# Kernel optimization log

Hardware: AMD Instinct MI355X
Metric: run time of the kernel (lower is better)

The kernel has to match this reference:

```python
import jax, jax.numpy as jnp
import numpy as np

VOCAB, D, H = 32000, 4096, 1024
B, S = 256, 256
LN_EPS = 1e-5


def setup_inputs() -> dict:
    key = jax.random.key(0)
    ks = jax.random.split(key, 8)
    return {
        "input_ids": jax.random.randint(ks[0], (B, S), 0, VOCAB),
        "attention_mask": jax.random.randint(ks[1], (B, S), 0, 2).astype(jnp.int32),
        "query_ids": jax.random.randint(ks[2], (1, S), 0, VOCAB),
        "query_mask": jax.random.randint(ks[3], (1, S), 0, 2).astype(jnp.int32),
        "embed": jax.random.normal(ks[4], (VOCAB, D), dtype=jnp.float32) * 0.02,
        "ln_g": jnp.ones((D,), jnp.float32),
        "ln_b": jnp.zeros((D,), jnp.float32),
        "kW1": jax.random.normal(ks[5], (H, D), dtype=jnp.float32) * 0.02,
        "kb1": jnp.zeros((H,), jnp.float32),
        "kW2": jax.random.normal(ks[6], (H, H), dtype=jnp.float32) * 0.02,
        "kb2": jnp.zeros((H,), jnp.float32),
        "qW1": jax.random.normal(ks[7], (H, D), dtype=jnp.float32) * 0.02,
        "qb1": jnp.zeros((H,), jnp.float32),
        "qW2": jax.random.normal(jax.random.fold_in(key, 99), (H, H), dtype=jnp.float32) * 0.02,
        "qb2": jnp.zeros((H,), jnp.float32),
        "k": 5,
    }


def _pool_norm(ids, mask, embed, ln_g, ln_b):
    # embedding gather -> masked mean pool -> LayerNorm
    h = embed[ids]                                  # [B, S, D]
    m = mask.astype(h.dtype)[..., None]             # [B, S, 1]
    pooled = (h * m).sum(axis=1) / (m.sum(axis=1) + 1e-9)  # [B, D]
    mu = pooled.mean(axis=-1, keepdims=True)
    var = ((pooled - mu) ** 2).mean(axis=-1, keepdims=True)
    return (pooled - mu) * jax.lax.rsqrt(var + LN_EPS) * ln_g + ln_b


def _mlp(x, W1, b1, W2, b2):
    return jax.nn.relu(x @ W1.T + b1) @ W2.T + b2


def reference(input_ids, attention_mask, query_ids, query_mask, embed, ln_g, ln_b,
              kW1, kb1, kW2, kb2, qW1, qb1, qW2, qb2, k):
    keys = _mlp(_pool_norm(input_ids, attention_mask, embed, ln_g, ln_b),
                kW1, kb1, kW2, kb2)                 # [B, H]
    query = _mlp(_pool_norm(query_ids, query_mask, embed, ln_g, ln_b),
                 qW1, qb1, qW2, qb2)                # [1, H]
    scores = jax.nn.sigmoid((query @ keys.T)[0])    # [B]
    vals, idx = jax.lax.top_k(scores, k)
    return vals, idx
```

## Files before the change

kernel.cpp:

```cpp
#include <hip/hip_runtime.h>
#include <math.h>

#define DD 4096
#define HH 1024
#define BB 256
#define SS 256

typedef unsigned long long u64;
typedef __attribute__((ext_vector_type(4))) short sv4;
typedef __attribute__((ext_vector_type(8))) short sv8;
typedef __attribute__((ext_vector_type(4))) float f32x4;

__device__ __forceinline__ unsigned short f2bf(float x) {
    union { float f; unsigned u; } c; c.f = x;
    unsigned r = c.u + 0x7FFFu + ((c.u >> 16) & 1u);
    return (unsigned short)(r >> 16);
}
__device__ __forceinline__ float bf2f(unsigned short h) {
    union { unsigned u; float f; } c; c.u = ((unsigned)h) << 16;
    return c.f;
}
__device__ __forceinline__ void split4(const float4& v, sv4& h, sv4& l) {
    unsigned short hx = f2bf(v.x), hy = f2bf(v.y), hz = f2bf(v.z), hw = f2bf(v.w);
    h.x = (short)hx; h.y = (short)hy; h.z = (short)hz; h.w = (short)hw;
    l.x = (short)f2bf(v.x - bf2f(hx)); l.y = (short)f2bf(v.y - bf2f(hy));
    l.z = (short)f2bf(v.z - bf2f(hz)); l.w = (short)f2bf(v.w - bf2f(hw));
}
__device__ __forceinline__ void split8(const float4& a, const float4& b,
                                       sv8& h, sv8& l) {
    sv4 h0, l0, h1, l1;
    split4(a, h0, l0);
    split4(b, h1, l1);
    h.s0 = h0.x; h.s1 = h0.y; h.s2 = h0.z; h.s3 = h0.w;
    h.s4 = h1.x; h.s5 = h1.y; h.s6 = h1.z; h.s7 = h1.w;
    l.s0 = l0.x; l.s1 = l0.y; l.s2 = l0.z; l.s3 = l0.w;
    l.s4 = l1.x; l.s5 = l1.y; l.s6 = l1.z; l.s7 = l1.w;
}

__global__ __launch_bounds__(256) void prep_kernel(
        const int* __restrict__ ids, const int* __restrict__ mask,
        const int* __restrict__ qids, const int* __restrict__ qmask,
        int* __restrict__ SortedOff, int* __restrict__ Count) {
    __shared__ int s_key[256];
    __shared__ int wofs[4];
    int b = blockIdx.x, t = threadIdx.x;
    const int* I = (b < BB) ? ids  + b * SS : qids;
    const int* M = (b < BB) ? mask + b * SS : qmask;
    int id = I[t], m = M[t];
    u64 bal = __ballot(m != 0);
    int lane = t & 63, w = t >> 6;
    if (lane == 0) wofs[w] = __popcll(bal);
    s_key[t] = 0x7FFFFFFF;
    __syncthreads();
    int off = 0;
    #pragma unroll
    for (int i = 0; i < 4; ++i) if (i < w) off += wofs[i];
    int total = wofs[0] + wofs[1] + wofs[2] + wofs[3];
    if (m) s_key[off + __popcll(bal & ((1ull << lane) - 1ull))] = id;
    __syncthreads();
    for (int k = 2; k <= 256; k <<= 1) {
        for (int j = k >> 1; j > 0; j >>= 1) {
            int p = t ^ j;
            int a = s_key[t], c = s_key[p];
            bool dir = ((t & k) == 0);
            bool keepMin = ((t < p) == dir);
            int nv = keepMin ? (a < c ? a : c) : (a > c ? a : c);
            __syncthreads();
            s_key[t] = nv;
            __syncthreads();
        }
    }
    SortedOff[b * 256 + t] = (t < total) ? s_key[t] * DD : 0;
    if (t == 0) Count[b] = total;
}

__global__ __launch_bounds__(64) void pool_kernel(
        const int* __restrict__ SortedOff, const int* __restrict__ Count,
        const float* __restrict__ embed, float* __restrict__ Pooled) {
    __shared__ int s_off[256];
    int bid = blockIdx.x, t = threadIdx.x;
    int doc = bid >> 4, slice = bid & 15;
    int total = Count[doc];
    #pragma unroll
    for (int i = 0; i < 4; ++i) s_off[t + i * 64] = SortedOff[doc * 256 + t + i * 64];
    __syncthreads();
    float inv = 1.0f / ((float)total + 1e-9f);
    int col = (slice << 8) + (t << 2);
    const float* eb = embed + col;
    float ax = 0.f, ay = 0.f, az = 0.f, aw = 0.f;
    int j = 0;
    for (; j + 8 <= total; j += 8) {
        const float4 r0 = *(const float4*)(eb + s_off[j + 0]);
        const float4 r1 = *(const float4*)(eb + s_off[j + 1]);
        const float4 r2 = *(const float4*)(eb + s_off[j + 2]);
        const float4 r3 = *(const float4*)(eb + s_off[j + 3]);
        const float4 r4 = *(const float4*)(eb + s_off[j + 4]);
        const float4 r5 = *(const float4*)(eb + s_off[j + 5]);
        const float4 r6 = *(const float4*)(eb + s_off[j + 6]);
        const float4 r7 = *(const float4*)(eb + s_off[j + 7]);
        ax += ((r0.x + r1.x) + (r2.x + r3.x)) + ((r4.x + r5.x) + (r6.x + r7.x));
        ay += ((r0.y + r1.y) + (r2.y + r3.y)) + ((r4.y + r5.y) + (r6.y + r7.y));
        az += ((r0.z + r1.z) + (r2.z + r3.z)) + ((r4.z + r5.z) + (r6.z + r7.z));
        aw += ((r0.w + r1.w) + (r2.w + r3.w)) + ((r4.w + r5.w) + (r6.w + r7.w));
    }
    for (; j < total; ++j) {
        const float4 r0 = *(const float4*)(eb + s_off[j]);
        ax += r0.x; ay += r0.y; az += r0.z; aw += r0.w;
    }
    *(float4*)(Pooled + (size_t)doc * DD + col) =
        make_float4(ax * inv, ay * inv, az * inv, aw * inv);
}

__global__ __launch_bounds__(256) void ln_split_kernel(
        const float* __restrict__ Pooled, const float* __restrict__ g,
        const float* __restrict__ bb, short* __restrict__ Xh,
        short* __restrict__ Xl, float* __restrict__ Xq) {
    __shared__ float lds4[4];
    int b = blockIdx.x, t = threadIdx.x;
    const float* row = Pooled + (size_t)b * DD;
    float4 v[4];
    float s = 0.f;
    #pragma unroll
    for (int i = 0; i < 4; ++i) {
        v[i] = *(const float4*)(row + (t << 2) + (i << 10));
        s += (v[i].x + v[i].y) + (v[i].z + v[i].w);
    }
    #pragma unroll
    for (int o = 32; o; o >>= 1) s += __shfl_down(s, o);
    int lane = t & 63, w = t >> 6;
    if (lane == 0) lds4[w] = s;
    __syncthreads();
    float mu = (lds4[0] + lds4[1] + lds4[2] + lds4[3]) * (1.0f / DD);
    float q = 0.f;
    #pragma unroll
    for (int i = 0; i < 4; ++i) {
        float dx = v[i].x - mu, dy = v[i].y - mu, dz = v[i].z - mu, dw = v[i].w - mu;
        q += (dx * dx + dy * dy) + (dz * dz + dw * dw);
    }
    __syncthreads();
    #pragma unroll
    for (int o = 32; o; o >>= 1) q += __shfl_down(q, o);
    if (lane == 0) lds4[w] = q;
    __syncthreads();
    float var = (lds4[0] + lds4[1] + lds4[2] + lds4[3]) * (1.0f / DD);
    float sc = 1.0f / sqrtf(var + 1e-5f);
    #pragma unroll
    for (int i = 0; i < 4; ++i) {
        int col = (t << 2) + (i << 10);
        float4 gg = *(const float4*)(g + col);
        float4 bv = *(const float4*)(bb + col);
        float4 o4;
        o4.x = (v[i].x - mu) * sc * gg.x + bv.x;
        o4.y = (v[i].y - mu) * sc * gg.y + bv.y;
        o4.z = (v[i].z - mu) * sc * gg.z + bv.z;
        o4.w = (v[i].w - mu) * sc * gg.w + bv.w;
        if (b < BB) {
            sv4 h, l; split4(o4, h, l);
            *(sv4*)(Xh + (size_t)b * DD + col) = h;
            *(sv4*)(Xl + (size_t)b * DD + col) = l;
        } else {
            *(float4*)(Xq + col) = o4;
        }
    }
}

template <bool CONTRIB>
__device__ void gemm_mfma(
        const short* __restrict__ Ah, const short* __restrict__ Al,
        const float* __restrict__ Wf,
        int ldK, int m0, int n0, int kBase, int Kc, int N,
        float* __restrict__ Pout,
        const float* __restrict__ Qv, float* __restrict__ Contrib, int slot) {
    __shared__ short sAh[128 * 40] __attribute__((aligned(16)));
    __shared__ short sAl[128 * 40] __attribute__((aligned(16)));
    __shared__ short sBh[128 * 40] __attribute__((aligned(16)));
    __shared__ short sBl[128 * 40] __attribute__((aligned(16)));
    int tid = threadIdx.x;
    int lane = tid & 63, wv = tid >> 6;
    int wr = wv >> 1, wc = wv & 1;
    int l15 = lane & 15, grp = lane >> 4, lk = grp << 3;
    int srow = tid >> 1, soff = (tid & 1) << 4;
    f32x4 zero = {0.f, 0.f, 0.f, 0.f};
    f32x4 acc[4][4];
    #pragma unroll
    for (int i = 0; i < 4; ++i)
        #pragma unroll
        for (int j = 0; j < 4; ++j) acc[i][j] = zero;

    for (int k0 = 0; k0 < Kc; k0 += 32) {
        int gk = kBase + k0;
        size_t ga = (size_t)(m0 + srow) * ldK + gk + soff;
        sv8 vah0 = *(const sv8*)(Ah + ga);
        sv8 vah1 = *(const sv8*)(Ah + ga + 8);
        sv8 val0 = *(const sv8*)(Al + ga);
        sv8 val1 = *(const sv8*)(Al + ga + 8);
        const float* wp = Wf + (size_t)(n0 + srow) * ldK + gk + soff;
        float4 w0 = *(const float4*)(wp);
        float4 w1 = *(const float4*)(wp + 4);
        float4 w2 = *(const float4*)(wp + 8);
        float4 w3 = *(const float4*)(wp + 12);
        sv8 bh0, bl0, bh1, bl1;
        split8(w0, w1, bh0, bl0);
        split8(w2, w3, bh1, bl1);
        __syncthreads();
        int so = srow * 40 + soff;
        *(sv8*)(sAh + so) = vah0; *(sv8*)(sAh + so + 8) = vah1;
        *(sv8*)(sAl + so) = val0; *(sv8*)(sAl + so + 8) = val1;
        *(sv8*)(sBh + so) = bh0;  *(sv8*)(sBh + so + 8) = bh1;
        *(sv8*)(sBl + so) = bl0;  *(sv8*)(sBl + so + 8) = bl1;
        __syncthreads();
        sv8 fah[4], fal[4], fbh[4], fbl[4];
        #pragma unroll
        for (int i = 0; i < 4; ++i) {
            int ra = (wr * 64 + i * 16 + l15) * 40 + lk;
            int rb = (wc * 64 + i * 16 + l15) * 40 + lk;
            fah[i] = *(const sv8*)(sAh + ra);
            fal[i] = *(const sv8*)(sAl + ra);
            fbh[i] = *(const sv8*)(sBh + rb);
            fbl[i] = *(const sv8*)(sBl + rb);
        }
        #pragma unroll
        for (int i = 0; i < 4; ++i)
            #pragma unroll
            for (int j = 0; j < 4; ++j) {
                acc[i][j] = __builtin_amdgcn_mfma_f32_16x16x32_bf16(fah[i], fbh[j], acc[i][j], 0, 0, 0);
                acc[i][j] = __builtin_amdgcn_mfma_f32_16x16x32_bf16(fah[i], fbl[j], acc[i][j], 0, 0, 0);
                acc[i][j] = __builtin_amdgcn_mfma_f32_16x16x32_bf16(fal[i], fbh[j], acc[i][j], 0, 0, 0);
            }
    }

    if (CONTRIB) {
        float qv[4];
        #pragma unroll
        for (int j = 0; j < 4; ++j) qv[j] = Qv[n0 + wc * 64 + j * 16 + l15];
        #pragma unroll
        for (int i = 0; i < 4; ++i)
            #pragma unroll
            for (int r = 0; r < 4; ++r) {
                float s = acc[i][0][r] * qv[0] + acc[i][1][r] * qv[1]
                        + acc[i][2][r] * qv[2] + acc[i][3][r] * qv[3];
                s += __shfl_xor(s, 1); s += __shfl_xor(s, 2);
                s += __shfl_xor(s, 4); s += __shfl_xor(s, 8);
                if (l15 == 0) {
                    int row = m0 + wr * 64 + i * 16 + grp * 4 + r;
                    Contrib[(size_t)row * 256 + slot * 2 + wc] = s;
                }
            }
    } else {
        #pragma unroll
        for (int i = 0; i < 4; ++i)
            #pragma unroll
            for (int r = 0; r < 4; ++r) {
                int row = m0 + wr * 64 + i * 16 + grp * 4 + r;
                #pragma unroll
                for (int j = 0; j < 4; ++j)
                    Pout[(size_t)row * N + n0 + wc * 64 + j * 16 + l15] = acc[i][j][r];
            }
    }
}

__global__ __launch_bounds__(256) void layer1_kernel(
        const short* __restrict__ Xh, const short* __restrict__ Xl,
        const float* __restrict__ kW1,
        float* __restrict__ P1, const float* __restrict__ Xq,
        const float* __restrict__ qW1, const float* __restrict__ qb1,
        float* __restrict__ H1q) {
    int bid = blockIdx.x;
    if (bid < 256) {
        int z = bid & 15, nb = (bid >> 4) & 7, mb = bid >> 7;
        gemm_mfma<false>(Xh, Xl, kW1, DD, mb * 128, nb * 128, z * 256, 256,
                         HH, P1 + (size_t)z * BB * HH, nullptr, nullptr, 0);
    } else {
        int i = bid - 256, wv = threadIdx.x >> 6, lane = threadIdx.x & 63;
        int n = (i << 2) + wv;
        const float* wrow = qW1 + (size_t)n * DD;
        float s = 0.f;
        #pragma unroll
        for (int jj = 0; jj < 16; ++jj) {
            int k = jj * 256 + (lane << 2);
            float4 a = *(const float4*)(Xq + k);
            float4 ww = *(const float4*)(wrow + k);
            s += (a.x * ww.x + a.y * ww.y) + (a.z * ww.z + a.w * ww.w);
        }
        #pragma unroll
        for (int o = 32; o; o >>= 1) s += __shfl_down(s, o);
        if (lane == 0) H1q[n] = fmaxf(s + qb1[n], 0.f);
    }
}

__global__ __launch_bounds__(256) void reduce1_kernel(
        const float* __restrict__ P1, const float* __restrict__ kb1,
        short* __restrict__ H1h, short* __restrict__ H1l,
        const float* __restrict__ H1q, const float* __restrict__ qW2,
        const float* __restrict__ qb2, float* __restrict__ Qv) {
    int bid = blockIdx.x, t = threadIdx.x;
    if (bid < 256) {
        int col = t << 2;
        const float* base = P1 + (size_t)bid * HH + col;
        float4 s = *(const float4*)(kb1 + col);
        #pragma unroll
        for (int z = 0; z < 16; ++z) {
            float4 p = *(const float4*)(base + (size_t)z * BB * HH);
            s.x += p.x; s.y += p.y; s.z += p.z; s.w += p.w;
        }
        s.x = fmaxf(s.x, 0.f); s.y = fmaxf(s.y, 0.f);
        s.z = fmaxf(s.z, 0.f); s.w = fmaxf(s.w, 0.f);
        sv4 h, l; split4(s, h, l);
        size_t o = (size_t)bid * HH + col;
        *(sv4*)(H1h + o) = h;
        *(sv4*)(H1l + o) = l;
    } else {
        int i = bid - 256, wv = t >> 6, lane = t & 63;
        int n = (i << 2) + wv;
        const float* wrow = qW2 + (size_t)n * HH;
        float s = 0.f;
        #pragma unroll
        for (int jj = 0; jj < 4; ++jj) {
            int k = jj * 256 + (lane << 2);
            float4 a = *(const float4*)(H1q + k);
            float4 ww = *(const float4*)(wrow + k);
            s += (a.x * ww.x + a.y * ww.y) + (a.z * ww.z + a.w * ww.w);
        }
        #pragma unroll
        for (int o = 32; o; o >>= 1) s += __shfl_down(s, o);
        if (lane == 0) Qv[n] = s + qb2[n];
    }
}

__global__ __launch_bounds__(256) void layer2_kernel(
        const short* __restrict__ H1h, const short* __restrict__ H1l,
        const float* __restrict__ kW2,
        const float* __restrict__ Qv, float* __restrict__ Contrib) {
    int bid = blockIdx.x;
    int z = bid & 15, nb = (bid >> 4) & 7, mb = bid >> 7;
    gemm_mfma<true>(H1h, H1l, kW2, HH, mb * 128, nb * 128, z * 64, 64,
                    HH, nullptr, Qv, Contrib, z * 8 + nb);
}

__global__ __launch_bounds__(1024) void final_kernel(
        const float* __restrict__ Contrib, const float* __restrict__ kb2,
        const float* __restrict__ Qv, const int* __restrict__ kptr,
        float* __restrict__ out) {
    __shared__ float red[16];
    __shared__ float ss[BB];
    __shared__ float rv[16];
    __shared__ int   ri[16];
    __shared__ float s_bq;
    int t = threadIdx.x, lane = t & 63, w = t >> 6;
    float v = kb2[t] * Qv[t];
    #pragma unroll
    for (int o = 32; o; o >>= 1) v += __shfl_down(v, o);
    if (lane == 0) red[w] = v;
    __syncthreads();
    if (t == 0) {
        float b = 0.f;
        #pragma unroll
        for (int i = 0; i < 16; ++i) b += red[i];
        s_bq = b;
    }
    __syncthreads();
    if (t < BB) {
        const float* c = Contrib + (size_t)t * 256;
        float sx = 0.f, sy = 0.f, sz = 0.f, sw = 0.f;
        for (int j = 0; j < 256; j += 4) {
            float4 e = *(const float4*)(c + j);
            sx += e.x; sy += e.y; sz += e.z; sw += e.w;
        }
        float lg = s_bq + ((sx + sy) + (sz + sw));
        ss[t] = 1.0f / (1.0f + expf(-lg));
    }
    __syncthreads();
    int k = kptr[0];
    if (k > BB) k = BB;
    for (int i = 0; i < k; ++i) {
        float vv = (t < BB) ? ss[t] : -3.3e38f;
        int vi = t;
        #pragma unroll
        for (int o = 32; o; o >>= 1) {
            float ov = __shfl_down(vv, o);
            int   oi = __shfl_down(vi, o);
            if (ov > vv || (ov == vv && oi < vi)) { vv = ov; vi = oi; }
        }
        if (lane == 0) { rv[w] = vv; ri[w] = vi; }
        __syncthreads();
        if (t == 0) {
            float bv = rv[0]; int bi = ri[0];
            #pragma unroll
            for (int j = 1; j < 16; ++j)
                if (rv[j] > bv || (rv[j] == bv && ri[j] < bi)) { bv = rv[j]; bi = ri[j]; }
            out[i]     = bv;
            out[k + i] = (float)bi;
            ss[bi] = -3.0e38f;
        }
        __syncthreads();
    }
}

extern "C" void kernel_launch(void* const* d_in, const int* in_sizes, int n_in,
                              void* d_out, int out_size, void* d_ws, size_t ws_size,
                              hipStream_t stream) {
    const int*   input_ids  = (const int*)d_in[0];
    const int*   attn_mask  = (const int*)d_in[1];
    const int*   query_ids  = (const int*)d_in[2];
    const int*   query_mask = (const int*)d_in[3];
    const float* embed      = (const float*)d_in[4];
    const float* ln_g       = (const float*)d_in[5];
    const float* ln_b       = (const float*)d_in[6];
    const float* kW1        = (const float*)d_in[7];
    const float* kb1        = (const float*)d_in[8];
    const float* kW2        = (const float*)d_in[9];
    const float* kb2        = (const float*)d_in[10];
    const float* qW1        = (const float*)d_in[11];
    const float* qb1        = (const float*)d_in[12];
    const float* qW2        = (const float*)d_in[13];
    const float* qb2        = (const float*)d_in[14];
    const int*   kptr       = (const int*)d_in[15];

    char* p = (char*)d_ws;
    auto carve = [&](size_t bytes) {
        char* r = p;
        p += (bytes + 255) & ~(size_t)255;
        return r;
    };
    int*   SortedOff = (int*)carve((size_t)257 * 256 * 4);
    int*   Count     = (int*)carve((size_t)257 * 4);
    float* Pooled    = (float*)carve((size_t)257 * DD * 4);
    float* Xq        = (float*)carve((size_t)DD * 4);
    short* Xh        = (short*)carve((size_t)BB * DD * 2);
    short* Xl        = (short*)carve((size_t)BB * DD * 2);
    float* P1        = (float*)carve((size_t)16 * BB * HH * 4);
    float* H1q       = (float*)carve((size_t)HH * 4);
    short* H1h       = (short*)carve((size_t)BB * HH * 2);
    short* H1l       = (short*)carve((size_t)BB * HH * 2);
    float* Qv        = (float*)carve((size_t)HH * 4);
    float* Contrib   = (float*)carve((size_t)BB * 256 * 4);

    prep_kernel<<<257, 256, 0, stream>>>(input_ids, attn_mask, query_ids,
                                         query_mask, SortedOff, Count);
    pool_kernel<<<4112, 64, 0, stream>>>(SortedOff, Count, embed, Pooled);
    ln_split_kernel<<<257, 256, 0, stream>>>(Pooled, ln_g, ln_b, Xh, Xl, Xq);
    layer1_kernel<<<512, 256, 0, stream>>>(Xh, Xl, kW1, P1, Xq, qW1, qb1, H1q);
    reduce1_kernel<<<512, 256, 0, stream>>>(P1, kb1, H1h, H1l, H1q, qW2, qb2, Qv);
    layer2_kernel<<<256, 256, 0, stream>>>(H1h, H1l, kW2, Qv, Contrib);
    final_kernel<<<1, 1024, 0, stream>>>(Contrib, kb2, Qv, kptr, (float*)d_out);
}
```

Before: 141.0 us.

## Fuse token compaction/sort into pooling kernel, dropping the prep launch

Merges the mask-compaction and bitonic sort of token ids into the pooling kernel, so each pooling block sorts its own document's ids in LDS and reads the embedding rows directly. This removes one kernel launch and the global round trip for the sorted offsets and counts. The cost is that each document's sort now runs four times, once in each of the four column-slice blocks. Blocks also grow to 256 threads over 1024 columns, giving fewer, larger blocks (1028 instead of 4112), which changes parallelism in the gather.

```diff
diff --git a/kernel.cpp b/kernel.cpp
--- a/kernel.cpp
+++ b/kernel.cpp
@@ -37,15 +37,16 @@
     l.s4 = l1.x; l.s5 = l1.y; l.s6 = l1.z; l.s7 = l1.w;
 }
 
-__global__ __launch_bounds__(256) void prep_kernel(
+__global__ __launch_bounds__(256) void pool_kernel(
         const int* __restrict__ ids, const int* __restrict__ mask,
         const int* __restrict__ qids, const int* __restrict__ qmask,
-        int* __restrict__ SortedOff, int* __restrict__ Count) {
+        const float* __restrict__ embed, float* __restrict__ Pooled) {
     __shared__ int s_key[256];
     __shared__ int wofs[4];
-    int b = blockIdx.x, t = threadIdx.x;
-    const int* I = (b < BB) ? ids  + b * SS : qids;
-    const int* M = (b < BB) ? mask + b * SS : qmask;
+    int bid = blockIdx.x, t = threadIdx.x;
+    int doc = bid >> 2, slice = bid & 3;
+    const int* I = (doc < BB) ? ids  + doc * SS : qids;
+    const int* M = (doc < BB) ? mask + doc * SS : qmask;
     int id = I[t], m = M[t];
     u64 bal = __ballot(m != 0);
     int lane = t & 63, w = t >> 6;
@@ -70,41 +71,31 @@
             __syncthreads();
         }
     }
-    SortedOff[b * 256 + t] = (t < total) ? s_key[t] * DD : 0;
-    if (t == 0) Count[b] = total;
-}
-
-__global__ __launch_bounds__(64) void pool_kernel(
-        const int* __restrict__ SortedOff, const int* __restrict__ Count,
-        const float* __restrict__ embed, float* __restrict__ Pooled) {
-    __shared__ int s_off[256];
-    int bid = blockIdx.x, t = threadIdx.x;
-    int doc = bid >> 4, slice = bid & 15;
-    int total = Count[doc];
-    #pragma unroll
-    for (int i = 0; i < 4; ++i) s_off[t + i * 64] = SortedOff[doc * 256 + t + i * 64];
-    __syncthreads();
+    if (t < total) s_key[t] *= DD;
+    else s_key[t] = 0;
+    __syncthreads();
+
     float inv = 1.0f / ((float)total + 1e-9f);
-    int col = (slice << 8) + (t << 2);
+    int col = (slice << 10) + (t << 2);
     const float* eb = embed + col;
     float ax = 0.f, ay = 0.f, az = 0.f, aw = 0.f;
     int j = 0;
     for (; j + 8 <= total; j += 8) {
-        const float4 r0 = *(const float4*)(eb + s_off[j + 0]);
-        const float4 r1 = *(const float4*)(eb + s_off[j + 1]);
-        const float4 r2 = *(const float4*)(eb + s_off[j + 2]);
-        const float4 r3 = *(const float4*)(eb + s_off[j + 3]);
-        const float4 r4 = *(const float4*)(eb + s_off[j + 4]);
-        const float4 r5 = *(const float4*)(eb + s_off[j + 5]);
-        const float4 r6 = *(const float4*)(eb + s_off[j + 6]);
-        const float4 r7 = *(const float4*)(eb + s_off[j + 7]);
+        const float4 r0 = *(const float4*)(eb + s_key[j + 0]);
+        const float4 r1 = *(const float4*)(eb + s_key[j + 1]);
+        const float4 r2 = *(const float4*)(eb + s_key[j + 2]);
+        const float4 r3 = *(const float4*)(eb + s_key[j + 3]);
+        const float4 r4 = *(const float4*)(eb + s_key[j + 4]);
+        const float4 r5 = *(const float4*)(eb + s_key[j + 5]);
+        const float4 r6 = *(const float4*)(eb + s_key[j + 6]);
+        const float4 r7 = *(const float4*)(eb + s_key[j + 7]);
         ax += ((r0.x + r1.x) + (r2.x + r3.x)) + ((r4.x + r5.x) + (r6.x + r7.x));
         ay += ((r0.y + r1.y) + (r2.y + r3.y)) + ((r4.y + r5.y) + (r6.y + r7.y));
         az += ((r0.z + r1.z) + (r2.z + r3.z)) + ((r4.z + r5.z) + (r6.z + r7.z));
         aw += ((r0.w + r1.w) + (r2.w + r3.w)) + ((r4.w + r5.w) + (r6.w + r7.w));
     }
     for (; j < total; ++j) {
-        const float4 r0 = *(const float4*)(eb + s_off[j]);
+        const float4 r0 = *(const float4*)(eb + s_key[j]);
         ax += r0.x; ay += r0.y; az += r0.z; aw += r0.w;
     }
     *(float4*)(Pooled + (size_t)doc * DD + col) =
@@ -422,8 +413,6 @@
         p += (bytes + 255) & ~(size_t)255;
         return r;
     };
-    int*   SortedOff = (int*)carve((size_t)257 * 256 * 4);
-    int*   Count     = (int*)carve((size_t)257 * 4);
     float* Pooled    = (float*)carve((size_t)257 * DD * 4);
     float* Xq        = (float*)carve((size_t)DD * 4);
     short* Xh        = (short*)carve((size_t)BB * DD * 2);
@@ -431,13 +420,12 @@
     float* P1        = (float*)carve((size_t)16 * BB * HH * 4);
     float* H1q       = (float*)carve((size_t)HH * 4);
     short* H1h       = (short*)carve((size_t)BB * HH * 2);
-    short* H1l       = (short*)carve((size_t)BB * HH * 2);
+    short* H1l      = (short*)carve((size_t)BB * HH * 2);
     float* Qv        = (float*)carve((size_t)HH * 4);
     float* Contrib   = (float*)carve((size_t)BB * 256 * 4);
 
-    prep_kernel<<<257, 256, 0, stream>>>(input_ids, attn_mask, query_ids,
-                                         query_mask, SortedOff, Count);
-    pool_kernel<<<4112, 64, 0, stream>>>(SortedOff, Count, embed, Pooled);
+    pool_kernel<<<1028, 256, 0, stream>>>(input_ids, attn_mask, query_ids,
+                                          query_mask, embed, Pooled);
     ln_split_kernel<<<257, 256, 0, stream>>>(Pooled, ln_g, ln_b, Xh, Xl, Xq);
     layer1_kernel<<<512, 256, 0, stream>>>(Xh, Xl, kW1, P1, Xq, qW1, qb1, H1q);
     reduce1_kernel<<<512, 256, 0, stream>>>(P1, kb1, H1h, H1l, H1q, qW2, qb2, Qv);
```

After: 148.2 us. 1.05x slower.

## Fuse LayerNorm into pooling partial stats and layer1 GEMM A-load

Applied to the files above, without the earlier changes.

Removes the separate LayerNorm/split kernel. The pooling kernel now also emits per-slice sum and sum-of-squares. The layer1 GEMM reads fp32 pooled rows, applies the normalization on the fly and does the bf16 hi/lo split before staging to LDS. The query path normalizes into shared memory itself. This saves one launch and the Xh/Xl round trip through global memory. In exchange, each N-tile block redoes the normalization and split work, the A loads double in size, and variance now uses E[x^2]-mu^2, which is less numerically stable.

```diff
diff --git a/kernel.cpp b/kernel.cpp
--- a/kernel.cpp
+++ b/kernel.cpp
@@ -76,7 +76,8 @@
 
 __global__ __launch_bounds__(64) void pool_kernel(
         const int* __restrict__ SortedOff, const int* __restrict__ Count,
-        const float* __restrict__ embed, float* __restrict__ Pooled) {
+        const float* __restrict__ embed, float* __restrict__ Pooled,
+        float* __restrict__ S1, float* __restrict__ S2) {
     __shared__ int s_off[256];
     int bid = blockIdx.x, t = threadIdx.x;
     int doc = bid >> 4, slice = bid & 15;
@@ -107,74 +108,33 @@
         const float4 r0 = *(const float4*)(eb + s_off[j]);
         ax += r0.x; ay += r0.y; az += r0.z; aw += r0.w;
     }
-    *(float4*)(Pooled + (size_t)doc * DD + col) =
-        make_float4(ax * inv, ay * inv, az * inv, aw * inv);
-}
-
-__global__ __launch_bounds__(256) void ln_split_kernel(
-        const float* __restrict__ Pooled, const float* __restrict__ g,
-        const float* __restrict__ bb, short* __restrict__ Xh,
-        short* __restrict__ Xl, float* __restrict__ Xq) {
-    __shared__ float lds4[4];
-    int b = blockIdx.x, t = threadIdx.x;
-    const float* row = Pooled + (size_t)b * DD;
-    float4 v[4];
-    float s = 0.f;
+    float4 res = make_float4(ax * inv, ay * inv, az * inv, aw * inv);
+    *(float4*)(Pooled + (size_t)doc * DD + col) = res;
+    float s1 = (res.x + res.y) + (res.z + res.w);
+    float s2 = (res.x * res.x + res.y * res.y) + (res.z * res.z + res.w * res.w);
     #pragma unroll
-    for (int i = 0; i < 4; ++i) {
-        v[i] = *(const float4*)(row + (t << 2) + (i << 10));
-        s += (v[i].x + v[i].y) + (v[i].z + v[i].w);
-    }
-    #pragma unroll
-    for (int o = 32; o; o >>= 1) s += __shfl_down(s, o);
-    int lane = t & 63, w = t >> 6;
-    if (lane == 0) lds4[w] = s;
-    __syncthreads();
-    float mu = (lds4[0] + lds4[1] + lds4[2] + lds4[3]) * (1.0f / DD);
-    float q = 0.f;
-    #pragma unroll
-    for (int i = 0; i < 4; ++i) {
-        float dx = v[i].x - mu, dy = v[i].y - mu, dz = v[i].z - mu, dw = v[i].w - mu;
-        q += (dx * dx + dy * dy) + (dz * dz + dw * dw);
-    }
-    __syncthreads();
-    #pragma unroll
-    for (int o = 32; o; o >>= 1) q += __shfl_down(q, o);
-    if (lane == 0) lds4[w] = q;
-    __syncthreads();
-    float var = (lds4[0] + lds4[1] + lds4[2] + lds4[3]) * (1.0f / DD);
-    float sc = 1.0f / sqrtf(var + 1e-5f);
-    #pragma unroll
-    for (int i = 0; i < 4; ++i) {
-        int col = (t << 2) + (i << 10);
-        float4 gg = *(const float4*)(g + col);
-        float4 bv = *(const float4*)(bb + col);
-        float4 o4;
-        o4.x = (v[i].x - mu) * sc * gg.x + bv.x;
-        o4.y = (v[i].y - mu) * sc * gg.y + bv.y;
-        o4.z = (v[i].z - mu) * sc * gg.z + bv.z;
-        o4.w = (v[i].w - mu) * sc * gg.w + bv.w;
-        if (b < BB) {
-            sv4 h, l; split4(o4, h, l);
-            *(sv4*)(Xh + (size_t)b * DD + col) = h;
-            *(sv4*)(Xl + (size_t)b * DD + col) = l;
-        } else {
-            *(float4*)(Xq + col) = o4;
-        }
-    }
-}
-
-template <bool CONTRIB>
+    for (int o = 32; o; o >>= 1) {
+        s1 += __shfl_down(s1, o);
+        s2 += __shfl_down(s2, o);
+    }
+    if (t == 0) {
+        S1[doc * 16 + slice] = s1;
+        S2[doc * 16 + slice] = s2;
+    }
+}
+
+template <bool LN_A, bool CONTRIB>
 __device__ void gemm_mfma(
+        short* sAh, short* sAl, short* sBh, short* sBl,
+        float* muS, float* scS, float* sg, float* sb,
+        const float* __restrict__ Af,
         const short* __restrict__ Ah, const short* __restrict__ Al,
+        const float* __restrict__ S1, const float* __restrict__ S2,
+        const float* __restrict__ ln_g, const float* __restrict__ ln_b,
         const float* __restrict__ Wf,
         int ldK, int m0, int n0, int kBase, int Kc, int N,
         float* __restrict__ Pout,
         const float* __restrict__ Qv, float* __restrict__ Contrib, int slot) {
-    __shared__ short sAh[128 * 40] __attribute__((aligned(16)));
-    __shared__ short sAl[128 * 40] __attribute__((aligned(16)));
-    __shared__ short sBh[128 * 40] __attribute__((aligned(16)));
-    __shared__ short sBl[128 * 40] __attribute__((aligned(16)));
     int tid = threadIdx.x;
     int lane = tid & 63, wv = tid >> 6;
     int wr = wv >> 1, wc = wv & 1;
@@ -187,13 +147,72 @@
         #pragma unroll
         for (int j = 0; j < 4; ++j) acc[i][j] = zero;
 
+    if (LN_A) {
+        if (tid < 128) {
+            int row = m0 + tid;
+            float a1 = 0.f, a2 = 0.f;
+            #pragma unroll
+            for (int s = 0; s < 16; ++s) {
+                a1 += S1[row * 16 + s];
+                a2 += S2[row * 16 + s];
+            }
+            float mu = a1 * (1.0f / DD);
+            float var = a2 * (1.0f / DD) - mu * mu;
+            muS[tid] = mu;
+            scS[tid] = 1.0f / sqrtf(var + 1e-5f);
+        }
+        for (int i = tid; i < Kc; i += 256) {
+            sg[i] = ln_g[kBase + i];
+            sb[i] = ln_b[kBase + i];
+        }
+        __syncthreads();
+    }
+
     for (int k0 = 0; k0 < Kc; k0 += 32) {
         int gk = kBase + k0;
-        size_t ga = (size_t)(m0 + srow) * ldK + gk + soff;
-        sv8 vah0 = *(const sv8*)(Ah + ga);
-        sv8 vah1 = *(const sv8*)(Ah + ga + 8);
-        sv8 val0 = *(const sv8*)(Al + ga);
-        sv8 val1 = *(const sv8*)(Al + ga + 8);
+        sv8 vah0, vah1, val0, val1;
+        if (LN_A) {
+            size_t ga = (size_t)(m0 + srow) * ldK + gk + soff;
+            float4 p0 = *(const float4*)(Af + ga);
+            float4 p1 = *(const float4*)(Af + ga + 4);
+            float4 p2 = *(const float4*)(Af + ga + 8);
+            float4 p3 = *(const float4*)(Af + ga + 12);
+            float mu = muS[srow], scv = scS[srow];
+            int lkk = k0 + soff;
+            float4 g0 = *(const float4*)(sg + lkk);
+            float4 g1 = *(const float4*)(sg + lkk + 4);
+            float4 g2 = *(const float4*)(sg + lkk + 8);
+            float4 g3 = *(const float4*)(sg + lkk + 12);
+            float4 b0 = *(const float4*)(sb + lkk);
+            float4 b1 = *(const float4*)(sb + lkk + 4);
+            float4 b2 = *(const float4*)(sb + lkk + 8);
+            float4 b3 = *(const float4*)(sb + lkk + 12);
+            float4 o0, o1, o2, o3;
+            o0.x = (p0.x - mu) * scv * g0.x + b0.x;
+            o0.y = (p0.y - mu) * scv * g0.y + b0.y;
+            o0.z = (p0.z - mu) * scv * g0.z + b0.z;
+            o0.w = (p0.w - mu) * scv * g0.w + b0.w;
+            o1.x = (p1.x - mu) * scv * g1.x + b1.x;
+            o1.y = (p1.y - mu) * scv * g1.y + b1.y;
+            o1.z = (p1.z - mu) * scv * g1.z + b1.z;
+            o1.w = (p1.w - mu) * scv * g1.w + b1.w;
+            o2.x = (p2.x - mu) * scv * g2.x + b2.x;
+            o2.y = (p2.y - mu) * scv * g2.y + b2.y;
+            o2.z = (p2.z - mu) * scv * g2.z + b2.z;
+            o2.w = (p2.w - mu) * scv * g2.w + b2.w;
+            o3.x = (p3.x - mu) * scv * g3.x + b3.x;
+            o3.y = (p3.y - mu) * scv * g3.y + b3.y;
+            o3.z = (p3.z - mu) * scv * g3.z + b3.z;
+            o3.w = (p3.w - mu) * scv * g3.w + b3.w;
+            split8(o0, o1, vah0, val0);
+            split8(o2, o3, vah1, val1);
+        } else {
+            size_t ga = (size_t)(m0 + srow) * ldK + gk + soff;
+            vah0 = *(const sv8*)(Ah + ga);
+            vah1 = *(const sv8*)(Ah + ga + 8);
+            val0 = *(const sv8*)(Al + ga);
+            val1 = *(const sv8*)(Al + ga + 8);
+        }
         const float* wp = Wf + (size_t)(n0 + srow) * ldK + gk + soff;
         float4 w0 = *(const float4*)(wp);
         float4 w1 = *(const float4*)(wp + 4);
@@ -260,25 +279,60 @@
 }
 
 __global__ __launch_bounds__(256) void layer1_kernel(
-        const short* __restrict__ Xh, const short* __restrict__ Xl,
-        const float* __restrict__ kW1,
-        float* __restrict__ P1, const float* __restrict__ Xq,
+        const float* __restrict__ Pooled,
+        const float* __restrict__ S1, const float* __restrict__ S2,
+        const float* __restrict__ ln_g, const float* __restrict__ ln_b,
+        const float* __restrict__ kW1, float* __restrict__ P1,
         const float* __restrict__ qW1, const float* __restrict__ qb1,
         float* __restrict__ H1q) {
-    int bid = blockIdx.x;
+    __shared__ char smem[44032] __attribute__((aligned(16)));
+    int bid = blockIdx.x, t = threadIdx.x;
     if (bid < 256) {
+        short* sAh = (short*)smem;
+        short* sAl = (short*)(smem + 10240);
+        short* sBh = (short*)(smem + 20480);
+        short* sBl = (short*)(smem + 30720);
+        float* muS = (float*)(smem + 40960);
+        float* scS = (float*)(smem + 41472);
+        float* sg  = (float*)(smem + 41984);
+        float* sb  = (float*)(smem + 43008);
         int z = bid & 15, nb = (bid >> 4) & 7, mb = bid >> 7;
-        gemm_mfma<false>(Xh, Xl, kW1, DD, mb * 128, nb * 128, z * 256, 256,
-                         HH, P1 + (size_t)z * BB * HH, nullptr, nullptr, 0);
+        gemm_mfma<true, false>(sAh, sAl, sBh, sBl, muS, scS, sg, sb,
+                               Pooled, nullptr, nullptr, S1, S2, ln_g, ln_b,
+                               kW1, DD, mb * 128, nb * 128, z * 256, 256,
+                               HH, P1 + (size_t)z * BB * HH, nullptr, nullptr, 0);
     } else {
-        int i = bid - 256, wv = threadIdx.x >> 6, lane = threadIdx.x & 63;
+        float* qx = (float*)smem;
+        int i = bid - 256, wv = t >> 6, lane = t & 63;
+        float a1 = 0.f, a2 = 0.f;
+        #pragma unroll
+        for (int s = 0; s < 16; ++s) {
+            a1 += S1[BB * 16 + s];
+            a2 += S2[BB * 16 + s];
+        }
+        float mu = a1 * (1.0f / DD);
+        float sc = 1.0f / sqrtf(a2 * (1.0f / DD) - mu * mu + 1e-5f);
+        const float* qrow = Pooled + (size_t)BB * DD;
+        for (int k = t; k < 1024; k += 256) {
+            int c = k << 2;
+            float4 pv = *(const float4*)(qrow + c);
+            float4 gv = *(const float4*)(ln_g + c);
+            float4 bv = *(const float4*)(ln_b + c);
+            float4 ov;
+            ov.x = (pv.x - mu) * sc * gv.x + bv.x;
+            ov.y = (pv.y - mu) * sc * gv.y + bv.y;
+            ov.z = (pv.z - mu) * sc * gv.z + bv.z;
+            ov.w = (pv.w - mu) * sc * gv.w + bv.w;
+            *(float4*)(qx + c) = ov;
+        }
+        __syncthreads();
         int n = (i << 2) + wv;
         const float* wrow = qW1 + (size_t)n * DD;
         float s = 0.f;
         #pragma unroll
         for (int jj = 0; jj < 16; ++jj) {
             int k = jj * 256 + (lane << 2);
-            float4 a = *(const float4*)(Xq + k);
+            float4 a = *(const float4*)(qx + k);
             float4 ww = *(const float4*)(wrow + k);
             s += (a.x * ww.x + a.y * ww.y) + (a.z * ww.z + a.w * ww.w);
         }
@@ -331,10 +385,17 @@
         const short* __restrict__ H1h, const short* __restrict__ H1l,
         const float* __restrict__ kW2,
         const float* __restrict__ Qv, float* __restrict__ Contrib) {
+    __shared__ char smem[40960] __attribute__((aligned(16)));
+    short* sAh = (short*)smem;
+    short* sAl = (short*)(smem + 10240);
+    short* sBh = (short*)(smem + 20480);
+    short* sBl = (short*)(smem + 30720);
     int bid = blockIdx.x;
     int z = bid & 15, nb = (bid >> 4) & 7, mb = bid >> 7;
-    gemm_mfma<true>(H1h, H1l, kW2, HH, mb * 128, nb * 128, z * 64, 64,
-                    HH, nullptr, Qv, Contrib, z * 8 + nb);
+    gemm_mfma<false, true>(sAh, sAl, sBh, sBl, nullptr, nullptr, nullptr, nullptr,
+                           nullptr, H1h, H1l, nullptr, nullptr, nullptr, nullptr,
+                           kW2, HH, mb * 128, nb * 128, z * 64, 64,
+                           HH, nullptr, Qv, Contrib, z * 8 + nb);
 }
 
 __global__ __launch_bounds__(1024) void final_kernel(
@@ -425,9 +486,8 @@
     int*   SortedOff = (int*)carve((size_t)257 * 256 * 4);
     int*   Count     = (int*)carve((size_t)257 * 4);
     float* Pooled    = (float*)carve((size_t)257 * DD * 4);
-    float* Xq        = (float*)carve((size_t)DD * 4);
-    short* Xh        = (short*)carve((size_t)BB * DD * 2);
-    short* Xl        = (short*)carve((size_t)BB * DD * 2);
+    float* S1        = (float*)carve((size_t)257 * 16 * 4);
+    float* S2        = (float*)carve((size_t)257 * 16 * 4);
     float* P1        = (float*)carve((size_t)16 * BB * HH * 4);
     float* H1q       = (float*)carve((size_t)HH * 4);
     short* H1h       = (short*)carve((size_t)BB * HH * 2);
@@ -437,9 +497,9 @@
 
     prep_kernel<<<257, 256, 0, stream>>>(input_ids, attn_mask, query_ids,
                                          query_mask, SortedOff, Count);
-    pool_kernel<<<4112, 64, 0, stream>>>(SortedOff, Count, embed, Pooled);
-    ln_split_kernel<<<257, 256, 0, stream>>>(Pooled, ln_g, ln_b, Xh, Xl, Xq);
-    layer1_kernel<<<512, 256, 0, stream>>>(Xh, Xl, kW1, P1, Xq, qW1, qb1, H1q);
+    pool_kernel<<<4112, 64, 0, stream>>>(SortedOff, Count, embed, Pooled, S1, S2);
+    layer1_kernel<<<512, 256, 0, stream>>>(Pooled, S1, S2, ln_g, ln_b,
+                                           kW1, P1, qW1, qb1, H1q);
     reduce1_kernel<<<512, 256, 0, stream>>>(P1, kb1, H1h, H1l, H1q, qW2, qb2, Qv);
     layer2_kernel<<<256, 256, 0, stream>>>(H1h, H1l, kW2, Qv, Contrib);
     final_kernel<<<1, 1024, 0, stream>>>(Contrib, kb2, Qv, kptr, (float*)d_out);
```

Measured after the change: 136.7 us. 1.03x faster.
